# Performance work log

Measured on AMD Instinct MI355X. Metric: run time of the kernel, lower is better.

The kernel has to match this reference:

```python
import jax, jax.numpy as jnp
import numpy as np

K = 3
S = 1
C_IN = 64
C_OUT = 128

def setup_inputs() -> dict:
    key = jax.random.key(0)
    k1, k2, k3 = jax.random.split(key, 3)
    x = jax.random.normal(k1, (16, C_IN, 256, 256), dtype=jnp.float32)
    weight = jax.random.normal(k2, (C_OUT, C_IN, K, K), dtype=jnp.float32)
    bias = jax.random.normal(k3, (C_OUT,), dtype=jnp.float32)
    return {"x": x, "weight": weight, "bias": bias}

def reference(x, weight, bias):
    # SAME-style padding of k//2 on each side, stride S, output h//S x w//S
    pad = K // 2
    out = jax.lax.conv_general_dilated(
        x, weight,
        window_strides=(S, S),
        padding=[(pad, pad), (pad, pad)],
        dimension_numbers=("NCHW", "OIHW", "NCHW"),
    )
    return out + bias[None, :, None, None]
```

## Files before the change

### kernel.cpp

```cpp
#include <hip/hip_runtime.h>


typedef _Float16 half8_t __attribute__((ext_vector_type(8)));
typedef float floatx4 __attribute__((ext_vector_type(4)));

#define HH 256
#define WW 256
#define CIN 64
#define COUT 128
#define NB 16

#define XP_RSTRIDE   16512
#define XP_NSTRIDE   4260096
#define XP_RSTRIDE_B 33024
#define ROW_LDS      8448
#define TILE_BYTES   50688
#define TILE_UNITS   3168

__device__ inline void gload_lds16(const void* g, void* l) {
    __builtin_amdgcn_global_load_lds(
        (const __attribute__((address_space(1))) unsigned int*)g,
        (__attribute__((address_space(3))) unsigned int*)l, 16, 0, 0);
}

__global__ void Conv2d_wprep_kernel(const float* __restrict__ w, _Float16* __restrict__ w_t) {
    int idx = blockIdx.x * 256 + threadIdx.x;
    if (idx >= 9 * 8 * 128 * 8) return;
    const int j = idx & 7, cout = (idx >> 3) & 127, s = (idx >> 10) & 7, t = idx >> 13;
    w_t[idx] = (_Float16)w[(cout * 64 + s * 8 + j) * 9 + t];
}

__global__ void Conv2d_xpad_zero_kernel(_Float16* __restrict__ xp) {
    const int idx = blockIdx.x * 256 + threadIdx.x;
    const int n = blockIdx.y;
    if (idx >= 8224) return;
    size_t off;
    if (idx < 2064)      off = (size_t)idx * 8;
    else if (idx < 4128) off = (size_t)257 * XP_RSTRIDE + (size_t)(idx - 2064) * 8;
    else if (idx < 6176) { const int t = idx - 4128;
        off = (size_t)(1 + (t >> 3)) * XP_RSTRIDE + (size_t)(t & 7) * 8; }
    else { const int t = idx - 6176;
        off = (size_t)(1 + (t >> 3)) * XP_RSTRIDE + 257 * 64 + (size_t)(t & 7) * 8; }
    int4 z = {0, 0, 0, 0};
    *(int4*)(xp + (size_t)n * XP_NSTRIDE + off) = z;
}

__global__ __launch_bounds__(256) void Conv2d_xprep_kernel(const float* __restrict__ x,
                                                           _Float16* __restrict__ xp) {
    const int tid = threadIdx.x;
    const int u = tid & 7, colq = tid >> 3;
    const int n = blockIdx.z, h = blockIdx.y;
    const int col0 = blockIdx.x * 128 + colq * 4;

    float4 in[8];
#pragma unroll
    for (int j = 0; j < 8; ++j)
        in[j] = *(const float4*)(x + ((size_t)((n * 64 + u * 8 + j) * 256 + h) * 256) + col0);

    _Float16* dst = xp + (size_t)n * XP_NSTRIDE + (size_t)(h + 1) * XP_RSTRIDE +
                    (size_t)(col0 + 1) * 64 + u * 8;
#pragma unroll
    for (int i = 0; i < 4; ++i) {
        half8_t hv;
#pragma unroll
        for (int j = 0; j < 8; ++j) hv[j] = (_Float16)((const float*)&in[j])[i];
        *(half8_t*)(dst + (size_t)i * 64) = hv;
    }
}

__global__ __launch_bounds__(512, 2) void Conv2dManual_77695958385099_kernel(
    const _Float16* __restrict__ xp, const _Float16* __restrict__ w_t,
    const float* __restrict__ bias, float* __restrict__ out) {
    __shared__ __align__(16) unsigned char xs[2 * TILE_BYTES];
    const int tid = threadIdx.x;
    const int l = tid & 63, wv = tid >> 6;
    const int wq = wv >> 1;
    const int wp = wv & 1;
    const int g = l >> 4, ln = l & 15;
    const int ow0 = blockIdx.x * 64;
    const int band = blockIdx.y;
    const int n = blockIdx.z;

    const char* wl = (const char*)w_t + g * 2048 + (wq * 32 + ln) * 16;
    half8_t A[2][2][9];
#pragma unroll
    for (int cf = 0; cf < 2; ++cf)
#pragma unroll
        for (int h = 0; h < 2; ++h)
#pragma unroll
            for (int tp = 0; tp < 9; ++tp)
                A[cf][h][tp] = *(const half8_t*)(wl + cf * 256 + h * 8192 + tp * 16384);

    floatx4 bvv[2];
#pragma unroll
    for (int cf = 0; cf < 2; ++cf)
#pragma unroll
        for (int r = 0; r < 4; ++r) bvv[cf][r] = bias[wq * 32 + cf * 16 + g * 4 + r];

    const char* xbase = (const char*)xp + (size_t)n * XP_NSTRIDE * 2 + (size_t)ow0 * 128;

#define STAGE(BUFSEL, IT)                                                              \
    {                                                                                  \
        const char* gt = xbase + (size_t)(band * 64 + (IT) * 4) * XP_RSTRIDE_B;        \
        const unsigned lb = (BUFSEL) * TILE_BYTES;                                     \
        _Pragma("unroll")                                                              \
        for (int p = 0; p < 6; ++p) {                                                  \
            const int u = p * 512 + tid;                                               \
            int row = (p * 512) / 528;                                                 \
            if (u >= (row + 1) * 528) row++;                                           \
            const int rem = u - row * 528;                                             \
            const int c = rem >> 3, s = rem & 7;                                       \
            gload_lds16(gt + (size_t)row * XP_RSTRIDE_B + c * 128 +                    \
                            (((s ^ (c & 7))) << 4),                                    \
                        xs + lb + ((unsigned)(p * 512 + (tid & ~63)) << 4));           \
        }                                                                              \
        if (tid < 96) {                                                                \
            const int rem = 432 + tid;                                                 \
            const int c = rem >> 3, s = rem & 7;                                       \
            const int4 v = *(const int4*)(gt + (size_t)5 * XP_RSTRIDE_B + c * 128 +    \
                                          ((s ^ (c & 7)) << 4));                       \
            *(int4*)(xs + lb + (unsigned)(3072 + tid) * 16) = v;                       \
        }                                                                              \
    }

    STAGE(0, 0);
    __syncthreads();

    int cur = 0;
    for (int it = 0; it < 16; ++it) {
        if (it < 15) STAGE(cur ^ 1, it + 1);

        floatx4 acc[2][8];
#pragma unroll
        for (int cf = 0; cf < 2; ++cf)
#pragma unroll
            for (int pf = 0; pf < 8; ++pf) acc[cf][pf] = bvv[cf];

        const unsigned char* bb = xs + cur * TILE_BYTES;
#pragma unroll
        for (int kx = 0; kx < 3; ++kx)
#pragma unroll
            for (int h = 0; h < 2; ++h)
#pragma unroll
                for (int cg = 0; cg < 2; ++cg) {
                    const int c = wp * 32 + cg * 16 + kx + ln;
                    const unsigned char* bp = bb + c * 128 + (((4 * h + g) ^ (c & 7)) << 4);
#pragma unroll
                    for (int t = 0; t < 6; ++t) {
                        const half8_t bt = *(const half8_t*)(bp + t * ROW_LDS);
#pragma unroll
                        for (int ky = 0; ky < 3; ++ky) {
                            const int rr = t - ky;
                            if (rr >= 0 && rr < 4) {
                                acc[0][rr * 2 + cg] = __builtin_amdgcn_mfma_f32_16x16x32_f16(
                                    A[0][h][ky * 3 + kx], bt, acc[0][rr * 2 + cg], 0, 0, 0);
                                acc[1][rr * 2 + cg] = __builtin_amdgcn_mfma_f32_16x16x32_f16(
                                    A[1][h][ky * 3 + kx], bt, acc[1][rr * 2 + cg], 0, 0, 0);
                            }
                        }
                    }
                }

        __syncthreads();

        float* ob = out + ((size_t)(n * 128 + wq * 32 + g * 4)) * 65536 +
                    (size_t)(band * 64 + it * 4) * 256 + ow0 + wp * 32 + ln;
#pragma unroll
        for (int cf = 0; cf < 2; ++cf)
#pragma unroll
            for (int rr = 0; rr < 4; ++rr)
#pragma unroll
                for (int r = 0; r < 4; ++r)
#pragma unroll
                    for (int cg = 0; cg < 2; ++cg)
                        __builtin_nontemporal_store(
                            acc[cf][rr * 2 + cg][r],
                            ob + (size_t)(cf * 16 + r) * 65536 + rr * 256 + cg * 16);

        cur ^= 1;
    }
#undef STAGE
}

__global__ __launch_bounds__(256) void Conv2d_fallback_kernel(
    const float* __restrict__ x, const float* __restrict__ w,
    const float* __restrict__ bias, float* __restrict__ out) {
    const int tx = threadIdx.x & 15, ty = threadIdx.x >> 4;
    const int ow0 = blockIdx.x * 64 + tx * 4;
    const int oh = blockIdx.y * 16 + ty;
    const int gg = blockIdx.z & 7, n = blockIdx.z >> 3;
    const int co = gg * 16;
    float acc[16][4];
#pragma unroll
    for (int c = 0; c < 16; ++c) {
        const float b = bias[co + c];
#pragma unroll
        for (int p = 0; p < 4; ++p) acc[c][p] = b;
    }
    const float* xn = x + (size_t)n * CIN * HH * WW;
    const float* wb = w + (size_t)co * CIN * 9;
    for (int ci = 0; ci < CIN; ++ci) {
        const float* xc = xn + (size_t)ci * HH * WW;
        float in[3][6];
#pragma unroll
        for (int ky = 0; ky < 3; ++ky) {
            const int iy = oh + ky - 1;
            if ((unsigned)iy < (unsigned)HH) {
                const float* row = xc + iy * WW;
                const float4 v = *(const float4*)(row + ow0);
                in[ky][1] = v.x; in[ky][2] = v.y; in[ky][3] = v.z; in[ky][4] = v.w;
                in[ky][0] = (ow0 > 0) ? row[ow0 - 1] : 0.0f;
                in[ky][5] = (ow0 < WW - 4) ? row[ow0 + 4] : 0.0f;
            } else {
#pragma unroll
                for (int j = 0; j < 6; ++j) in[ky][j] = 0.0f;
            }
        }
        const float* wc2 = wb + ci * 9;
#pragma unroll
        for (int c = 0; c < 16; ++c) {
            const float* wcc = wc2 + (size_t)c * CIN * 9;
#pragma unroll
            for (int ky = 0; ky < 3; ++ky)
#pragma unroll
                for (int kx = 0; kx < 3; ++kx) {
                    const float wv2 = wcc[ky * 3 + kx];
#pragma unroll
                    for (int p = 0; p < 4; ++p) acc[c][p] += in[ky][kx + p] * wv2;
                }
        }
    }
    const size_t hw = (size_t)HH * WW;
    float* ob = out + ((size_t)n * COUT + co) * hw + (size_t)oh * WW + ow0;
#pragma unroll
    for (int c = 0; c < 16; ++c) {
        float4 v;
        v.x = acc[c][0]; v.y = acc[c][1]; v.z = acc[c][2]; v.w = acc[c][3];
        *(float4*)(ob + (size_t)c * hw) = v;
    }
}

extern "C" void kernel_launch(void* const* d_in, const int* in_sizes, int n_in,
                              void* d_out, int out_size, void* d_ws, size_t ws_size,
                              hipStream_t stream) {
    const float* x = (const float*)d_in[0];
    const float* w = (const float*)d_in[1];
    const float* b = (const float*)d_in[2];
    float* out = (float*)d_out;

    const size_t xp_bytes = (size_t)NB * XP_NSTRIDE * 2;
    const size_t wt_bytes = (size_t)9 * 8 * 128 * 8 * 2;

    if (ws_size >= xp_bytes + wt_bytes) {
        char* ws = (char*)d_ws;
        _Float16* xp = (_Float16*)ws;
        _Float16* w_t = (_Float16*)(ws + xp_bytes);
        Conv2d_wprep_kernel<<<dim3(288), 256, 0, stream>>>(w, w_t);
        Conv2d_xpad_zero_kernel<<<dim3(33, 16), 256, 0, stream>>>(xp);
        Conv2d_xprep_kernel<<<dim3(2, 256, 16), 256, 0, stream>>>(x, xp);
        Conv2dManual_77695958385099_kernel<<<dim3(4, 4, 16), 512, 0, stream>>>(
            xp, w_t, b, out);
    } else {
        dim3 grid(WW / 64, HH / 16, NB * (COUT / 16));
        Conv2d_fallback_kernel<<<grid, 256, 0, stream>>>(x, w, b, out);
    }
}
```

Measured before the change: 791.1 us.

## Remap waves to 16 output channels over full width, stage epilogue through LDS

Each wave now owns 16 output channels across all 64 columns instead of 32 channels by 32 columns. This halves the weight registers per wave and loads all six input rows per channel group once, reusing them across the ky taps. Output is transposed through a per-wave LDS scratch buffer so stores become 16-byte vectors. The end-of-iteration __syncthreads is replaced by a manual barrier whose vmcnt(16) wait lets the already-issued next-tile loads stay outstanding, with addresses precomputed. Risks include the wait-count being wrong for the actual number of in-flight loads, extra LDS capacity pressure, and ordering hazards between the scratch buffer and the barrier.

```diff
diff --git a/kernel.cpp b/kernel.cpp
--- a/kernel.cpp
+++ b/kernel.cpp
@@ -15,7 +15,6 @@
 #define XP_RSTRIDE_B 33024
 #define ROW_LDS      8448
 #define TILE_BYTES   50688
-#define TILE_UNITS   3168
 
 __device__ inline void gload_lds16(const void* g, void* l) {
     __builtin_amdgcn_global_load_lds(
@@ -72,30 +71,36 @@
     const _Float16* __restrict__ xp, const _Float16* __restrict__ w_t,
     const float* __restrict__ bias, float* __restrict__ out) {
     __shared__ __align__(16) unsigned char xs[2 * TILE_BYTES];
+    __shared__ __align__(16) float esc[8][1088];
     const int tid = threadIdx.x;
-    const int l = tid & 63, wv = tid >> 6;
-    const int wq = wv >> 1;
-    const int wp = wv & 1;
+    const int l = tid & 63, wvid = tid >> 6;
     const int g = l >> 4, ln = l & 15;
     const int ow0 = blockIdx.x * 64;
     const int band = blockIdx.y;
     const int n = blockIdx.z;
 
-    const char* wl = (const char*)w_t + g * 2048 + (wq * 32 + ln) * 16;
-    half8_t A[2][2][9];
-#pragma unroll
-    for (int cf = 0; cf < 2; ++cf)
-#pragma unroll
-        for (int h = 0; h < 2; ++h)
-#pragma unroll
-            for (int tp = 0; tp < 9; ++tp)
-                A[cf][h][tp] = *(const half8_t*)(wl + cf * 256 + h * 8192 + tp * 16384);
-
-    floatx4 bvv[2];
-#pragma unroll
-    for (int cf = 0; cf < 2; ++cf)
-#pragma unroll
-        for (int r = 0; r < 4; ++r) bvv[cf][r] = bias[wq * 32 + cf * 16 + g * 4 + r];
+    const char* wl = (const char*)w_t + g * 2048 + (wvid * 16 + ln) * 16;
+    half8_t A[2][9];
+#pragma unroll
+    for (int h = 0; h < 2; ++h)
+#pragma unroll
+        for (int tp = 0; tp < 9; ++tp)
+            A[h][tp] = *(const half8_t*)(wl + h * 8192 + tp * 16384);
+
+    floatx4 bv;
+#pragma unroll
+    for (int r = 0; r < 4; ++r) bv[r] = bias[wvid * 16 + g * 4 + r];
+
+    int F[4][3][2];
+#pragma unroll
+    for (int cgf = 0; cgf < 4; ++cgf)
+#pragma unroll
+        for (int kx = 0; kx < 3; ++kx)
+#pragma unroll
+            for (int h = 0; h < 2; ++h) {
+                const int c = cgf * 16 + kx + ln;
+                F[cgf][kx][h] = c * 128 + (((4 * h + g) ^ (c & 7)) << 4);
+            }
 
     const char* xbase = (const char*)xp + (size_t)n * XP_NSTRIDE * 2 + (size_t)ow0 * 128;
 
@@ -124,17 +129,20 @@
     }
 
     STAGE(0, 0);
-    __syncthreads();
+    asm volatile("s_waitcnt vmcnt(0) lgkmcnt(0)" ::: "memory");
+    __builtin_amdgcn_s_barrier();
+    __builtin_amdgcn_sched_barrier(0);
 
     int cur = 0;
+#pragma unroll 1
     for (int it = 0; it < 16; ++it) {
         if (it < 15) STAGE(cur ^ 1, it + 1);
 
-        floatx4 acc[2][8];
-#pragma unroll
-        for (int cf = 0; cf < 2; ++cf)
-#pragma unroll
-            for (int pf = 0; pf < 8; ++pf) acc[cf][pf] = bvv[cf];
+        floatx4 acc[4][4];
+#pragma unroll
+        for (int rr = 0; rr < 4; ++rr)
+#pragma unroll
+            for (int cgf = 0; cgf < 4; ++cgf) acc[rr][cgf] = bv;
 
         const unsigned char* bb = xs + cur * TILE_BYTES;
 #pragma unroll
@@ -142,41 +150,47 @@
 #pragma unroll
             for (int h = 0; h < 2; ++h)
 #pragma unroll
-                for (int cg = 0; cg < 2; ++cg) {
-                    const int c = wp * 32 + cg * 16 + kx + ln;
-                    const unsigned char* bp = bb + c * 128 + (((4 * h + g) ^ (c & 7)) << 4);
-#pragma unroll
-                    for (int t = 0; t < 6; ++t) {
-                        const half8_t bt = *(const half8_t*)(bp + t * ROW_LDS);
-#pragma unroll
-                        for (int ky = 0; ky < 3; ++ky) {
-                            const int rr = t - ky;
-                            if (rr >= 0 && rr < 4) {
-                                acc[0][rr * 2 + cg] = __builtin_amdgcn_mfma_f32_16x16x32_f16(
-                                    A[0][h][ky * 3 + kx], bt, acc[0][rr * 2 + cg], 0, 0, 0);
-                                acc[1][rr * 2 + cg] = __builtin_amdgcn_mfma_f32_16x16x32_f16(
-                                    A[1][h][ky * 3 + kx], bt, acc[1][rr * 2 + cg], 0, 0, 0);
-                            }
-                        }
+                for (int cgf = 0; cgf < 4; ++cgf) {
+                    const unsigned char* bp = bb + F[cgf][kx][h];
+                    half8_t bt[6];
+#pragma unroll
+                    for (int t = 0; t < 6; ++t)
+                        bt[t] = *(const half8_t*)(bp + t * ROW_LDS);
+#pragma unroll
+                    for (int ky = 0; ky < 3; ++ky) {
+                        const half8_t af = A[h][ky * 3 + kx];
+#pragma unroll
+                        for (int rr = 0; rr < 4; ++rr)
+                            acc[rr][cgf] = __builtin_amdgcn_mfma_f32_16x16x32_f16(
+                                af, bt[rr + ky], acc[rr][cgf], 0, 0, 0);
                     }
                 }
 
-        __syncthreads();
-
-        float* ob = out + ((size_t)(n * 128 + wq * 32 + g * 4)) * 65536 +
-                    (size_t)(band * 64 + it * 4) * 256 + ow0 + wp * 32 + ln;
-#pragma unroll
-        for (int cf = 0; cf < 2; ++cf)
-#pragma unroll
-            for (int rr = 0; rr < 4; ++rr)
+        float* scr = &esc[wvid][0];
+        const int orow0 = band * 64 + it * 4;
+        float* obase = out + ((size_t)(n * 128 + wvid * 16)) * 65536 +
+                       (size_t)orow0 * 256 + ow0;
+#pragma unroll
+        for (int rr = 0; rr < 4; ++rr) {
+#pragma unroll
+            for (int cgf = 0; cgf < 4; ++cgf)
 #pragma unroll
                 for (int r = 0; r < 4; ++r)
-#pragma unroll
-                    for (int cg = 0; cg < 2; ++cg)
-                        __builtin_nontemporal_store(
-                            acc[cf][rr * 2 + cg][r],
-                            ob + (size_t)(cf * 16 + r) * 65536 + rr * 256 + cg * 16);
-
+                    scr[(g * 4 + r) * 68 + cgf * 16 + ln] = acc[rr][cgf][r];
+#pragma unroll
+            for (int q = 0; q < 4; ++q) {
+                const int co = q * 4 + g;
+                const floatx4 v = *(const floatx4*)(scr + co * 68 + ln * 4);
+                __builtin_nontemporal_store(
+                    v, (floatx4*)(obase + (size_t)co * 65536 + rr * 256 + ln * 4));
+            }
+        }
+
+        if (it < 15) {
+            asm volatile("s_waitcnt vmcnt(16) lgkmcnt(0)" ::: "memory");
+            __builtin_amdgcn_s_barrier();
+            __builtin_amdgcn_sched_barrier(0);
+        }
         cur ^= 1;
     }
 #undef STAGE
```

After: 775.8 us. About the same (-1.9%).
